# Optimization experiments

Hardware: AMD Instinct MI355X
Metric: run time of the kernel (lower is better)

Reference implementation:

```python
import jax, jax.numpy as jnp
import numpy as np

D_MODEL = 1024
N_HEADS = 16
HEAD_DIM = D_MODEL // N_HEADS


def setup_inputs() -> dict:
    key = jax.random.key(0)
    ks = jax.random.split(key, 9)
    s = 1.0 / np.sqrt(D_MODEL)
    return {
        "x": jax.random.normal(ks[0], (4, 2048, D_MODEL), dtype=jnp.float32),
        "Wq": jax.random.normal(ks[1], (D_MODEL, D_MODEL), dtype=jnp.float32) * s,
        "bq": jax.random.normal(ks[2], (D_MODEL,), dtype=jnp.float32) * 0.01,
        "Wk": jax.random.normal(ks[3], (D_MODEL, D_MODEL), dtype=jnp.float32) * s,
        "bk": jax.random.normal(ks[4], (D_MODEL,), dtype=jnp.float32) * 0.01,
        "Wv": jax.random.normal(ks[5], (D_MODEL, D_MODEL), dtype=jnp.float32) * s,
        "bv": jax.random.normal(ks[6], (D_MODEL,), dtype=jnp.float32) * 0.01,
        "Wo": jax.random.normal(ks[7], (D_MODEL, D_MODEL), dtype=jnp.float32) * s,
        "bo": jax.random.normal(ks[8], (D_MODEL,), dtype=jnp.float32) * 0.01,
    }


def reference(x, Wq, bq, Wk, bk, Wv, bv, Wo, bo):
    b, s, d = x.shape  # [batch, seq, d_model]
    # projections (weights stored as [d_in, d_out], equiv to torch Linear W.T)
    q = x @ Wq + bq
    k = x @ Wk + bk
    v = x @ Wv + bv
    # split heads -> [b, h, s, hd]
    q = q.reshape(b, s, N_HEADS, HEAD_DIM).transpose(0, 2, 1, 3)
    k = k.reshape(b, s, N_HEADS, HEAD_DIM).transpose(0, 2, 1, 3)
    v = v.reshape(b, s, N_HEADS, HEAD_DIM).transpose(0, 2, 1, 3)
    scale = 1.0 / jnp.sqrt(jnp.asarray(HEAD_DIM, dtype=q.dtype))
    scores = jnp.einsum("bhqd,bhkd->bhqk", q, k) * scale  # [b,h,s,s]
    attn = jax.nn.softmax(scores, axis=-1)
    y = jnp.einsum("bhqk,bhkd->bhqd", attn, v)
    y = y.transpose(0, 2, 1, 3).reshape(b, s, d)
    return y @ Wo + bo
```

## Files before the change

### kernel.cpp

```cpp
#include <hip/hip_runtime.h>

#define SEQ   2048
#define DM    1024
#define NH    16
#define HD    64
#define MTOT  8192
#define QSCALE 0.18033688011112042f
#define SMAX  12.0f

typedef _Float16 f16x8 __attribute__((ext_vector_type(8)));
typedef float    f32x4 __attribute__((ext_vector_type(4)));

__device__ __forceinline__ unsigned short f2h(float f) {
    _Float16 h = (_Float16)f;
    return __builtin_bit_cast(unsigned short, h);
}
__device__ __forceinline__ float h2f(unsigned short u) {
    return (float)__builtin_bit_cast(_Float16, u);
}
__device__ __forceinline__ unsigned int pkrtz(float a, float b) {
    return __builtin_bit_cast(unsigned int, __builtin_amdgcn_cvt_pkrtz(a, b));
}
__device__ __forceinline__ float fexp2(float x) {
    return __builtin_amdgcn_exp2f(x);
}
__device__ __forceinline__ void async_cp16(const void* g, void* l) {
    __builtin_amdgcn_global_load_lds(
        (const __attribute__((address_space(1))) unsigned int*)g,
        (__attribute__((address_space(3))) unsigned int*)l, 16, 0, 0);
}

__global__ __launch_bounds__(256) void convert_x_kernel(
    const float* __restrict__ x, unsigned short* __restrict__ Xh)
{
    const size_t i8 = ((size_t)blockIdx.x * 256 + threadIdx.x) * 8;
    float f[8];
    *(float4*)&f[0] = *(const float4*)(x + i8);
    *(float4*)&f[4] = *(const float4*)(x + i8 + 4);
    unsigned short h[8];
#pragma unroll
    for (int e = 0; e < 8; ++e) h[e] = f2h(f[e]);
    uint4 ph;
    ph.x = h[0] | ((unsigned)h[1] << 16); ph.y = h[2] | ((unsigned)h[3] << 16);
    ph.z = h[4] | ((unsigned)h[5] << 16); ph.w = h[6] | ((unsigned)h[7] << 16);
    *(uint4*)(Xh + i8) = ph;
}

__global__ __launch_bounds__(256) void convert_w_kernel(
    const float* __restrict__ Wq, const float* __restrict__ Wk,
    const float* __restrict__ Wv, const float* __restrict__ Wo,
    unsigned short* __restrict__ WTh, unsigned short* __restrict__ WTl)
{
    __shared__ float tile[32][33];
    const int z = blockIdx.z;
    const float* W = (z == 0) ? Wq : (z == 1) ? Wk : (z == 2) ? Wv : Wo;
    const float s = (z == 0) ? QSCALE : 1.0f;
    const int r0 = blockIdx.y << 5, c0 = blockIdx.x << 5;
    const int tx = threadIdx.x, ty = threadIdx.y;
#pragma unroll
    for (int u = 0; u < 4; ++u)
        tile[ty + 8 * u][tx] = W[(size_t)(r0 + ty + 8 * u) * DM + c0 + tx];
    __syncthreads();
#pragma unroll
    for (int u = 0; u < 4; ++u) {
        const int dout = c0 + ty + 8 * u;
        const int din  = r0 + tx;
        const float v = tile[tx][ty + 8 * u] * s;
        const unsigned short hh = f2h(v);
        const size_t idx = (size_t)(z * DM + dout) * DM + din;
        WTh[idx] = hh;
        if (z == 3) WTl[idx] = f2h(v - h2f(hh));
    }
}

__global__ __launch_bounds__(256, 3) void gemm_kernel(
    const unsigned short* __restrict__ Agh, const unsigned short* __restrict__ Agl,
    const unsigned short* __restrict__ Bgh, const unsigned short* __restrict__ Bgl,
    const float* __restrict__ b0, const float* __restrict__ b1,
    const float* __restrict__ b2,
    float* __restrict__ Cf,
    unsigned short* __restrict__ Qf, unsigned short* __restrict__ Kf,
    unsigned short* __restrict__ Vt,
    const int mode)
{
    __shared__ unsigned short gsm[16384];

    const int t = threadIdx.x;
    const int wave = t >> 6, L = t & 63;
    const int quad = L >> 4, l16 = L & 15;
    const int m0 = blockIdx.x << 7, n0 = blockIdx.y << 7;

    const int trl = L >> 2;
    const int ck  = (L & 3) ^ (trl & 3);
    const unsigned short* gsrc;
    unsigned short* lb;
    int ub;
    if (mode == 1) {
        gsrc = (wave < 2) ? Agh : Bgh;
        ub   = (wave & 1) << 2;
        lb   = &gsm[((wave >> 1) << 13) + (ub << 9)];
    } else {
        gsrc = (wave == 0) ? Agh : (wave == 1) ? Agl
             : (wave == 2) ? Bgh : Bgl;
        ub   = 0;
        lb   = &gsm[wave << 12];
    }
    const int rbase = (wave < 2) ? m0 : n0;
    const unsigned short* gl = gsrc + (size_t)(rbase + trl) * DM + ck * 8;

    const int wm = (wave >> 1) << 6, wn = (wave & 1) << 6;
    const int xk2 = l16 & 3;
    f32x4 acc[4][4] = {};

    for (int k0 = 0; k0 < DM; k0 += 32) {
        __syncthreads();
        if (mode == 1) {
#pragma unroll
            for (int u = 0; u < 4; ++u)
                async_cp16(gl + (size_t)(ub + u) * 16 * DM + k0, lb + (u << 9));
        } else {
#pragma unroll
            for (int u = 0; u < 8; ++u)
                async_cp16(gl + (size_t)u * 16 * DM + k0, lb + (u << 9));
        }
        __syncthreads();

        f16x8 fah[4], fal[4], fbh[4], fbl[4];
#pragma unroll
        for (int i = 0; i < 4; ++i) {
            const int ao = (wm + (i << 4) + l16) * 32 + ((quad ^ xk2) << 3);
            fah[i] = *(const f16x8*)&gsm[ao];
        }
#pragma unroll
        for (int j = 0; j < 4; ++j) {
            const int bo_ = (wn + (j << 4) + l16) * 32 + ((quad ^ xk2) << 3);
            fbh[j] = *(const f16x8*)&gsm[8192 + bo_];
        }
        if (mode == 0) {
#pragma unroll
            for (int i = 0; i < 4; ++i) {
                const int ao = (wm + (i << 4) + l16) * 32 + ((quad ^ xk2) << 3);
                fal[i] = *(const f16x8*)&gsm[4096 + ao];
            }
#pragma unroll
            for (int j = 0; j < 4; ++j) {
                const int bo_ = (wn + (j << 4) + l16) * 32 + ((quad ^ xk2) << 3);
                fbl[j] = *(const f16x8*)&gsm[12288 + bo_];
            }
        }
#pragma unroll
        for (int i = 0; i < 4; ++i)
#pragma unroll
            for (int j = 0; j < 4; ++j) {
                acc[i][j] = __builtin_amdgcn_mfma_f32_16x16x32_f16(fah[i], fbh[j], acc[i][j], 0, 0, 0);
                if (mode == 0) {
                    acc[i][j] = __builtin_amdgcn_mfma_f32_16x16x32_f16(fal[i], fbh[j], acc[i][j], 0, 0, 0);
                    acc[i][j] = __builtin_amdgcn_mfma_f32_16x16x32_f16(fah[i], fbl[j], acc[i][j], 0, 0, 0);
                }
            }
    }

    if (mode == 0) {
#pragma unroll
        for (int j = 0; j < 4; ++j) {
            const int col = n0 + wn + (j << 4) + l16;
            const float bj = b0[col];
#pragma unroll
            for (int i = 0; i < 4; ++i)
#pragma unroll
                for (int r = 0; r < 4; ++r) {
                    const int row = m0 + wm + (i << 4) + (quad << 2) + r;
                    Cf[(size_t)row * DM + col] = acc[i][j][r] + bj;
                }
        }
    } else {
#pragma unroll
        for (int j = 0; j < 4; ++j) {
            const int col = n0 + wn + (j << 4) + l16;
            const int seg = col >> 10;
            const int c = col & 1023;
            const int h_ = c >> 6, d_ = c & 63;
            const float bj = (seg == 0) ? b0[c] * QSCALE : (seg == 1) ? b1[c] : b2[c];
            unsigned short* Op = (seg == 0) ? Qf : Kf;
#pragma unroll
            for (int i = 0; i < 4; ++i) {
                const int row0 = m0 + wm + (i << 4) + (quad << 2);
                const int b_ = row0 >> 11, s0 = row0 & 2047;
                if (seg < 2) {
                    const size_t ib = ((size_t)b_ * NH + h_) * SEQ;
#pragma unroll
                    for (int r = 0; r < 4; ++r)
                        Op[(ib + s0 + r) * HD + d_] = f2h(acc[i][j][r] + bj);
                } else {
                    unsigned short e[4];
#pragma unroll
                    for (int r = 0; r < 4; ++r) e[r] = f2h(acc[i][j][r] + bj);
                    const size_t idx = (((size_t)b_ * NH + h_) * HD + d_) * SEQ + s0;
                    uint2 pv;
                    pv.x = e[0] | ((unsigned)e[1] << 16);
                    pv.y = e[2] | ((unsigned)e[3] << 16);
                    *(uint2*)&Vt[idx] = pv;
                }
            }
        }
    }
}

__global__ __launch_bounds__(256, 4) void attn_kernel(
    const unsigned short* __restrict__ Qg,
    const unsigned short* __restrict__ Kg,
    const unsigned short* __restrict__ Vg,
    unsigned short* __restrict__ Yh, unsigned short* __restrict__ Yl)
{
    __shared__ unsigned short smem[16384];

    const int t = threadIdx.x;
    const int wave = t >> 6, L = t & 63;
    const int quad = L >> 4, l16 = L & 15;
    const int xk = l16 & 7;
    const int bh = blockIdx.x;
    const int q0 = blockIdx.y << 7;
    const size_t base = (size_t)bh * SEQ * HD;

    f16x8 fQ[2][2];
#pragma unroll
    for (int nt = 0; nt < 2; ++nt) {
        const size_t qr = (size_t)(q0 + (wave << 5) + (nt << 4) + l16);
#pragma unroll
        for (int ks = 0; ks < 2; ++ks)
            fQ[nt][ks] = *(const f16x8*)(Qg + base + qr * HD + (ks << 5) + (quad << 3));
    }

    const int trl = L >> 3;
    const int sck = (L & 7) ^ trl;
    const unsigned short* sg = (wave == 0) ? Kg : Vg;
    const size_t rstr = (wave == 1) ? (size_t)SEQ : (size_t)HD;
    const unsigned short* gbase = sg + base + trl * rstr + sck * 8;
    unsigned short* lb = &smem[wave << 12];

    float lsum[2] = {0.0f, 0.0f};
    f32x4 o[2][4] = {};

    for (int kt = 0; kt < 32; ++kt) {
        __syncthreads();
        if (wave < 2) {
            const size_t koff = (wave == 0) ? ((size_t)kt << 12) : ((size_t)kt << 6);
            const unsigned short* g = gbase + koff;
#pragma unroll
            for (int u = 0; u < 8; ++u)
                async_cp16(g + ((size_t)u << 3) * rstr, lb + (u << 9));
        }
        __syncthreads();

        f32x4 sacc[2][4];
#pragma unroll
        for (int nt = 0; nt < 2; ++nt)
#pragma unroll
            for (int mt = 0; mt < 4; ++mt)
                sacc[nt][mt] = (f32x4){-SMAX, -SMAX, -SMAX, -SMAX};
        __builtin_amdgcn_s_setprio(1);
#pragma unroll
        for (int mt = 0; mt < 4; ++mt) {
#pragma unroll
            for (int ks = 0; ks < 2; ++ks) {
                const int off = ((mt << 4) + l16) * 64 + ((((ks << 2) + quad) ^ xk) << 3);
                const f16x8 fK = *(const f16x8*)&smem[off];
#pragma unroll
                for (int nt = 0; nt < 2; ++nt)
                    sacc[nt][mt] = __builtin_amdgcn_mfma_f32_16x16x32_f16(fK, fQ[nt][ks], sacc[nt][mt], 0, 0, 0);
            }
        }
        __builtin_amdgcn_s_setprio(0);

#pragma unroll
        for (int nt = 0; nt < 2; ++nt) {
            const int prow = (wave << 5) + (nt << 4) + l16;
#pragma unroll
            for (int mt = 0; mt < 4; ++mt) {
                float p[4];
#pragma unroll
                for (int r = 0; r < 4; ++r) {
                    p[r] = fexp2(sacc[nt][mt][r]);
                    lsum[nt] += p[r];
                }
                uint2 pk;
                pk.x = pkrtz(p[0], p[1]);
                pk.y = pkrtz(p[2], p[3]);
                const int ch = ((mt << 1) + (quad >> 1)) ^ xk;
                *(uint2*)&smem[8192 + prow * 64 + (ch << 3) + ((quad & 1) << 2)] = pk;
            }
        }

        f16x8 fV[4][2];
#pragma unroll
        for (int dt = 0; dt < 4; ++dt)
#pragma unroll
            for (int ks = 0; ks < 2; ++ks) {
                const int off = 4096 + ((dt << 4) + l16) * 64 + ((((ks << 2) + quad) ^ xk) << 3);
                fV[dt][ks] = *(const f16x8*)&smem[off];
            }
#pragma unroll
        for (int nt = 0; nt < 2; ++nt) {
            const int prow = (wave << 5) + (nt << 4) + l16;
            f16x8 fP[2];
#pragma unroll
            for (int ks = 0; ks < 2; ++ks) {
                const int off = 8192 + prow * 64 + ((((ks << 2) + quad) ^ xk) << 3);
                fP[ks] = *(const f16x8*)&smem[off];
            }
            __builtin_amdgcn_s_setprio(1);
#pragma unroll
            for (int dt = 0; dt < 4; ++dt)
#pragma unroll
                for (int ks = 0; ks < 2; ++ks)
                    o[nt][dt] = __builtin_amdgcn_mfma_f32_16x16x32_f16(fP[ks], fV[dt][ks], o[nt][dt], 0, 0, 0);
            __builtin_amdgcn_s_setprio(0);
        }
    }

#pragma unroll
    for (int nt = 0; nt < 2; ++nt) {
        lsum[nt] += __shfl_xor(lsum[nt], 16);
        lsum[nt] += __shfl_xor(lsum[nt], 32);
    }
    const int b_ = bh >> 4, h_ = bh & 15;
#pragma unroll
    for (int nt = 0; nt < 2; ++nt) {
        const float linv = 1.0f / lsum[nt];
        float lr[4];
#pragma unroll
        for (int r = 0; r < 4; ++r) lr[r] = __shfl(linv, (quad << 2) + r);
#pragma unroll
        for (int dt = 0; dt < 4; ++dt)
#pragma unroll
            for (int r = 0; r < 4; ++r) {
                const int row = q0 + (wave << 5) + (nt << 4) + (quad << 2) + r;
                const float v = o[nt][dt][r] * lr[r];
                const size_t idx = ((size_t)b_ * SEQ + row) * DM + (h_ << 6) + (dt << 4) + l16;
                const unsigned short hh = f2h(v);
                Yh[idx] = hh;
                Yl[idx] = f2h(v - h2f(hh));
            }
    }
}

extern "C" void kernel_launch(void* const* d_in, const int* in_sizes, int n_in,
                              void* d_out, int out_size, void* d_ws, size_t ws_size,
                              hipStream_t stream)
{
    const float* x  = (const float*)d_in[0];
    const float* Wq = (const float*)d_in[1];
    const float* bq = (const float*)d_in[2];
    const float* Wk = (const float*)d_in[3];
    const float* bk = (const float*)d_in[4];
    const float* Wv = (const float*)d_in[5];
    const float* bv = (const float*)d_in[6];
    const float* Wo = (const float*)d_in[7];
    const float* bo = (const float*)d_in[8];
    float* out = (float*)d_out;

    char* w = (char*)d_ws;
    unsigned short* Xh  = (unsigned short*)(w);
    unsigned short* Yl  = (unsigned short*)(w + (16u << 20));
    unsigned short* Qf  = (unsigned short*)(w + (32u << 20));
    unsigned short* Kf  = (unsigned short*)(w + (48u << 20));
    unsigned short* Vt  = (unsigned short*)(w + (64u << 20));
    unsigned short* WTh = (unsigned short*)(w + (112u << 20));
    unsigned short* WTl = (unsigned short*)(w + (120u << 20));
    unsigned short* Yh = Xh;

    convert_x_kernel<<<dim3(MTOT * DM / (256 * 8)), dim3(256), 0, stream>>>(x, Xh);
    convert_w_kernel<<<dim3(32, 32, 4), dim3(32, 8), 0, stream>>>(Wq, Wk, Wv, Wo, WTh, WTl);

    gemm_kernel<<<dim3(64, 24), dim3(256), 0, stream>>>(
        Xh, nullptr, WTh, nullptr, bq, bk, bv,
        nullptr, Qf, Kf, Vt, 1);

    attn_kernel<<<dim3(4 * NH, SEQ / 128), dim3(256), 0, stream>>>(
        Qf, Kf, Vt, Yh, Yl);

    gemm_kernel<<<dim3(64, 8), dim3(256), 0, stream>>>(
        Yh, Yl, WTh + (size_t)3072 * DM, WTl + (size_t)3072 * DM,
        bo, nullptr, nullptr,
        out, nullptr, nullptr, nullptr, 0);
}
```

Baseline: 331.4 us.

## Double-buffer QKV GEMM loads and split attention across eight waves

The mode-1 (QKV projection) GEMM path now double-buffers its LDS tiles: it prefetches the next K-slice while computing the current one and drops one barrier per iteration, with setprio around the MFMA block. The attention kernel moves from 256 to 512 threads, so each wave handles 16 query rows instead of 32, which halves per-wave registers and accumulators. Waves 0 and 1 still stage K and V into shared memory. The intent is to hide global load latency in the GEMM and raise parallelism and latency tolerance in attention, at the cost of more waves contending for barriers and LDS per K tile.

```diff
diff --git a/kernel.cpp b/kernel.cpp
--- a/kernel.cpp
+++ b/kernel.cpp
@@ -93,17 +93,17 @@
     const int trl = L >> 2;
     const int ck  = (L & 3) ^ (trl & 3);
     const unsigned short* gsrc;
-    unsigned short* lb;
+    unsigned short* lbw;
     int ub;
     if (mode == 1) {
         gsrc = (wave < 2) ? Agh : Bgh;
         ub   = (wave & 1) << 2;
-        lb   = &gsm[((wave >> 1) << 13) + (ub << 9)];
+        lbw  = &gsm[((wave >> 1) << 13) + ((wave & 1) << 11)];
     } else {
         gsrc = (wave == 0) ? Agh : (wave == 1) ? Agl
              : (wave == 2) ? Bgh : Bgl;
         ub   = 0;
-        lb   = &gsm[wave << 12];
+        lbw  = &gsm[wave << 12];
     }
     const int rbase = (wave < 2) ? m0 : n0;
     const unsigned short* gl = gsrc + (size_t)(rbase + trl) * DM + ck * 8;
@@ -112,52 +112,70 @@
     const int xk2 = l16 & 3;
     f32x4 acc[4][4] = {};
 
-    for (int k0 = 0; k0 < DM; k0 += 32) {
-        __syncthreads();
-        if (mode == 1) {
-#pragma unroll
-            for (int u = 0; u < 4; ++u)
-                async_cp16(gl + (size_t)(ub + u) * 16 * DM + k0, lb + (u << 9));
-        } else {
-#pragma unroll
-            for (int u = 0; u < 8; ++u)
-                async_cp16(gl + (size_t)u * 16 * DM + k0, lb + (u << 9));
-        }
-        __syncthreads();
-
-        f16x8 fah[4], fal[4], fbh[4], fbl[4];
-#pragma unroll
-        for (int i = 0; i < 4; ++i) {
-            const int ao = (wm + (i << 4) + l16) * 32 + ((quad ^ xk2) << 3);
-            fah[i] = *(const f16x8*)&gsm[ao];
-        }
-#pragma unroll
-        for (int j = 0; j < 4; ++j) {
-            const int bo_ = (wn + (j << 4) + l16) * 32 + ((quad ^ xk2) << 3);
-            fbh[j] = *(const f16x8*)&gsm[8192 + bo_];
-        }
-        if (mode == 0) {
+    if (mode == 1) {
+#pragma unroll
+        for (int u = 0; u < 4; ++u)
+            async_cp16(gl + (size_t)(ub + u) * 16 * DM, lbw + (u << 9));
+
+        for (int k0 = 0; k0 < DM; k0 += 32) {
+            const int p = (k0 >> 5) & 1;
+            __syncthreads();
+            if (k0 < DM - 32) {
+#pragma unroll
+                for (int u = 0; u < 4; ++u)
+                    async_cp16(gl + (size_t)(ub + u) * 16 * DM + (k0 + 32),
+                               lbw + ((p ^ 1) << 12) + (u << 9));
+            }
+            const int pb = p << 12;
+            f16x8 fah[4], fbh[4];
 #pragma unroll
             for (int i = 0; i < 4; ++i) {
                 const int ao = (wm + (i << 4) + l16) * 32 + ((quad ^ xk2) << 3);
-                fal[i] = *(const f16x8*)&gsm[4096 + ao];
+                fah[i] = *(const f16x8*)&gsm[pb + ao];
             }
 #pragma unroll
             for (int j = 0; j < 4; ++j) {
                 const int bo_ = (wn + (j << 4) + l16) * 32 + ((quad ^ xk2) << 3);
+                fbh[j] = *(const f16x8*)&gsm[8192 + pb + bo_];
+            }
+            __builtin_amdgcn_s_setprio(1);
+#pragma unroll
+            for (int i = 0; i < 4; ++i)
+#pragma unroll
+                for (int j = 0; j < 4; ++j)
+                    acc[i][j] = __builtin_amdgcn_mfma_f32_16x16x32_f16(fah[i], fbh[j], acc[i][j], 0, 0, 0);
+            __builtin_amdgcn_s_setprio(0);
+        }
+    } else {
+        for (int k0 = 0; k0 < DM; k0 += 32) {
+            __syncthreads();
+#pragma unroll
+            for (int u = 0; u < 8; ++u)
+                async_cp16(gl + (size_t)u * 16 * DM + k0, lbw + (u << 9));
+            __syncthreads();
+
+            f16x8 fah[4], fal[4], fbh[4], fbl[4];
+#pragma unroll
+            for (int i = 0; i < 4; ++i) {
+                const int ao = (wm + (i << 4) + l16) * 32 + ((quad ^ xk2) << 3);
+                fah[i] = *(const f16x8*)&gsm[ao];
+                fal[i] = *(const f16x8*)&gsm[4096 + ao];
+            }
+#pragma unroll
+            for (int j = 0; j < 4; ++j) {
+                const int bo_ = (wn + (j << 4) + l16) * 32 + ((quad ^ xk2) << 3);
+                fbh[j] = *(const f16x8*)&gsm[8192 + bo_];
                 fbl[j] = *(const f16x8*)&gsm[12288 + bo_];
             }
-        }
-#pragma unroll
-        for (int i = 0; i < 4; ++i)
-#pragma unroll
-            for (int j = 0; j < 4; ++j) {
-                acc[i][j] = __builtin_amdgcn_mfma_f32_16x16x32_f16(fah[i], fbh[j], acc[i][j], 0, 0, 0);
-                if (mode == 0) {
+#pragma unroll
+            for (int i = 0; i < 4; ++i)
+#pragma unroll
+                for (int j = 0; j < 4; ++j) {
+                    acc[i][j] = __builtin_amdgcn_mfma_f32_16x16x32_f16(fah[i], fbh[j], acc[i][j], 0, 0, 0);
                     acc[i][j] = __builtin_amdgcn_mfma_f32_16x16x32_f16(fal[i], fbh[j], acc[i][j], 0, 0, 0);
                     acc[i][j] = __builtin_amdgcn_mfma_f32_16x16x32_f16(fah[i], fbl[j], acc[i][j], 0, 0, 0);
                 }
-            }
+        }
     }
 
     if (mode == 0) {
@@ -206,7 +224,7 @@
     }
 }
 
-__global__ __launch_bounds__(256, 4) void attn_kernel(
+__global__ __launch_bounds__(512, 8) void attn_kernel(
     const unsigned short* __restrict__ Qg,
     const unsigned short* __restrict__ Kg,
     const unsigned short* __restrict__ Vg,
@@ -222,24 +240,23 @@
     const int q0 = blockIdx.y << 7;
     const size_t base = (size_t)bh * SEQ * HD;
 
-    f16x8 fQ[2][2];
-#pragma unroll
-    for (int nt = 0; nt < 2; ++nt) {
-        const size_t qr = (size_t)(q0 + (wave << 5) + (nt << 4) + l16);
+    f16x8 fQ[2];
+    {
+        const size_t qr = (size_t)(q0 + (wave << 4) + l16);
 #pragma unroll
         for (int ks = 0; ks < 2; ++ks)
-            fQ[nt][ks] = *(const f16x8*)(Qg + base + qr * HD + (ks << 5) + (quad << 3));
+            fQ[ks] = *(const f16x8*)(Qg + base + qr * HD + (ks << 5) + (quad << 3));
     }
 
     const int trl = L >> 3;
     const int sck = (L & 7) ^ trl;
-    const unsigned short* sg = (wave == 0) ? Kg : Vg;
+    const unsigned short* sg = (wave == 1) ? Vg : Kg;
     const size_t rstr = (wave == 1) ? (size_t)SEQ : (size_t)HD;
     const unsigned short* gbase = sg + base + trl * rstr + sck * 8;
-    unsigned short* lb = &smem[wave << 12];
-
-    float lsum[2] = {0.0f, 0.0f};
-    f32x4 o[2][4] = {};
+    unsigned short* lb = &smem[(wave & 1) << 12];
+
+    float lsum = 0.0f;
+    f32x4 o[4] = {};
 
     for (int kt = 0; kt < 32; ++kt) {
         __syncthreads();
@@ -252,12 +269,10 @@
         }
         __syncthreads();
 
-        f32x4 sacc[2][4];
-#pragma unroll
-        for (int nt = 0; nt < 2; ++nt)
-#pragma unroll
-            for (int mt = 0; mt < 4; ++mt)
-                sacc[nt][mt] = (f32x4){-SMAX, -SMAX, -SMAX, -SMAX};
+        f32x4 sacc[4];
+#pragma unroll
+        for (int mt = 0; mt < 4; ++mt)
+            sacc[mt] = (f32x4){-SMAX, -SMAX, -SMAX, -SMAX};
         __builtin_amdgcn_s_setprio(1);
 #pragma unroll
         for (int mt = 0; mt < 4; ++mt) {
@@ -265,30 +280,25 @@
             for (int ks = 0; ks < 2; ++ks) {
                 const int off = ((mt << 4) + l16) * 64 + ((((ks << 2) + quad) ^ xk) << 3);
                 const f16x8 fK = *(const f16x8*)&smem[off];
-#pragma unroll
-                for (int nt = 0; nt < 2; ++nt)
-                    sacc[nt][mt] = __builtin_amdgcn_mfma_f32_16x16x32_f16(fK, fQ[nt][ks], sacc[nt][mt], 0, 0, 0);
+                sacc[mt] = __builtin_amdgcn_mfma_f32_16x16x32_f16(fK, fQ[ks], sacc[mt], 0, 0, 0);
             }
         }
         __builtin_amdgcn_s_setprio(0);
 
-#pragma unroll
-        for (int nt = 0; nt < 2; ++nt) {
-            const int prow = (wave << 5) + (nt << 4) + l16;
-#pragma unroll
-            for (int mt = 0; mt < 4; ++mt) {
-                float p[4];
-#pragma unroll
-                for (int r = 0; r < 4; ++r) {
-                    p[r] = fexp2(sacc[nt][mt][r]);
-                    lsum[nt] += p[r];
-                }
-                uint2 pk;
-                pk.x = pkrtz(p[0], p[1]);
-                pk.y = pkrtz(p[2], p[3]);
-                const int ch = ((mt << 1) + (quad >> 1)) ^ xk;
-                *(uint2*)&smem[8192 + prow * 64 + (ch << 3) + ((quad & 1) << 2)] = pk;
-            }
+        const int prow = (wave << 4) + l16;
+#pragma unroll
+        for (int mt = 0; mt < 4; ++mt) {
+            float p[4];
+#pragma unroll
+            for (int r = 0; r < 4; ++r) {
+                p[r] = fexp2(sacc[mt][r]);
+                lsum += p[r];
+            }
+            uint2 pk;
+            pk.x = pkrtz(p[0], p[1]);
+            pk.y = pkrtz(p[2], p[3]);
+            const int ch = ((mt << 1) + (quad >> 1)) ^ xk;
+            *(uint2*)&smem[8192 + prow * 64 + (ch << 3) + ((quad & 1) << 2)] = pk;
         }
 
         f16x8 fV[4][2];
@@ -299,49 +309,39 @@
                 const int off = 4096 + ((dt << 4) + l16) * 64 + ((((ks << 2) + quad) ^ xk) << 3);
                 fV[dt][ks] = *(const f16x8*)&smem[off];
             }
-#pragma unroll
-        for (int nt = 0; nt < 2; ++nt) {
-            const int prow = (wave << 5) + (nt << 4) + l16;
-            f16x8 fP[2];
-#pragma unroll
-            for (int ks = 0; ks < 2; ++ks) {
-                const int off = 8192 + prow * 64 + ((((ks << 2) + quad) ^ xk) << 3);
-                fP[ks] = *(const f16x8*)&smem[off];
-            }
-            __builtin_amdgcn_s_setprio(1);
-#pragma unroll
-            for (int dt = 0; dt < 4; ++dt)
-#pragma unroll
-                for (int ks = 0; ks < 2; ++ks)
-                    o[nt][dt] = __builtin_amdgcn_mfma_f32_16x16x32_f16(fP[ks], fV[dt][ks], o[nt][dt], 0, 0, 0);
-            __builtin_amdgcn_s_setprio(0);
-        }
-    }
-
-#pragma unroll
-    for (int nt = 0; nt < 2; ++nt) {
-        lsum[nt] += __shfl_xor(lsum[nt], 16);
-        lsum[nt] += __shfl_xor(lsum[nt], 32);
-    }
+        f16x8 fP[2];
+#pragma unroll
+        for (int ks = 0; ks < 2; ++ks) {
+            const int off = 8192 + prow * 64 + ((((ks << 2) + quad) ^ xk) << 3);
+            fP[ks] = *(const f16x8*)&smem[off];
+        }
+        __builtin_amdgcn_s_setprio(1);
+#pragma unroll
+        for (int dt = 0; dt < 4; ++dt)
+#pragma unroll
+            for (int ks = 0; ks < 2; ++ks)
+                o[dt] = __builtin_amdgcn_mfma_f32_16x16x32_f16(fP[ks], fV[dt][ks], o[dt], 0, 0, 0);
+        __builtin_amdgcn_s_setprio(0);
+    }
+
+    lsum += __shfl_xor(lsum, 16);
+    lsum += __shfl_xor(lsum, 32);
     const int b_ = bh >> 4, h_ = bh & 15;
-#pragma unroll
-    for (int nt = 0; nt < 2; ++nt) {
-        const float linv = 1.0f / lsum[nt];
-        float lr[4];
-#pragma unroll
-        for (int r = 0; r < 4; ++r) lr[r] = __shfl(linv, (quad << 2) + r);
-#pragma unroll
-        for (int dt = 0; dt < 4; ++dt)
-#pragma unroll
-            for (int r = 0; r < 4; ++r) {
-                const int row = q0 + (wave << 5) + (nt << 4) + (quad << 2) + r;
-                const float v = o[nt][dt][r] * lr[r];
-                const size_t idx = ((size_t)b_ * SEQ + row) * DM + (h_ << 6) + (dt << 4) + l16;
-                const unsigned short hh = f2h(v);
-                Yh[idx] = hh;
-                Yl[idx] = f2h(v - h2f(hh));
-            }
-    }
+    const float linv = 1.0f / lsum;
+    float lr[4];
+#pragma unroll
+    for (int r = 0; r < 4; ++r) lr[r] = __shfl(linv, (quad << 2) + r);
+#pragma unroll
+    for (int dt = 0; dt < 4; ++dt)
+#pragma unroll
+        for (int r = 0; r < 4; ++r) {
+            const int row = q0 + (wave << 4) + (quad << 2) + r;
+            const float v = o[dt][r] * lr[r];
+            const size_t idx = ((size_t)b_ * SEQ + row) * DM + (h_ << 6) + (dt << 4) + l16;
+            const unsigned short hh = f2h(v);
+            Yh[idx] = hh;
+            Yl[idx] = f2h(v - h2f(hh));
+        }
 }
 
 extern "C" void kernel_launch(void* const* d_in, const int* in_sizes, int n_in,
@@ -376,7 +376,7 @@
         Xh, nullptr, WTh, nullptr, bq, bk, bv,
         nullptr, Qf, Kf, Vt, 1);
 
-    attn_kernel<<<dim3(4 * NH, SEQ / 128), dim3(256), 0, stream>>>(
+    attn_kernel<<<dim3(4 * NH, SEQ / 128), dim3(512), 0, stream>>>(
         Qf, Kf, Vt, Yh, Yl);
 
     gemm_kernel<<<dim3(64, 8), dim3(256), 0, stream>>>(
```

After: 515.4 us. 1.55x slower.
